# Optimization experiments

Measured on AMD Instinct MI355X. Metric: run time of the kernel, lower is better.

## Reference

```python
import jax, jax.numpy as jnp
import numpy as np

B, N, E_PER_G = 32, 2048, 16384
NF, NHID, NCLS = 128, 128, 10
RATIO = 0.5
NT = B * N
E = B * E_PER_G
K1 = int(np.ceil(RATIO * N))        # 1024 nodes kept per graph after pool1
K2 = int(np.ceil(RATIO * K1))       # 512
K3 = int(np.ceil(RATIO * K2))       # 256


def setup_inputs() -> dict:
    key = jax.random.key(0)
    ks = jax.random.split(key, 16)
    x = jax.random.normal(ks[0], (NT, NF), dtype=jnp.float32)
    off = (jnp.arange(B, dtype=jnp.int32) * N)[:, None]
    src = (jax.random.randint(ks[1], (B, E_PER_G), 0, N, dtype=jnp.int32) + off).reshape(-1)
    dst = (jax.random.randint(ks[2], (B, E_PER_G), 0, N, dtype=jnp.int32) + off).reshape(-1)
    edge_index = jnp.stack([src, dst])
    batch = jnp.repeat(jnp.arange(B, dtype=jnp.int32), N)
    def lin(k, i, o):
        return jax.random.normal(k, (i, o), jnp.float32) / np.float32(np.sqrt(i))
    return {
        'x': x, 'edge_index': edge_index, 'batch': batch,
        'W1': lin(ks[3], NF, NHID), 'b1': jnp.zeros((NHID,), jnp.float32),
        'Wp1': lin(ks[4], NHID, 1), 'bp1': jnp.zeros((1,), jnp.float32),
        'W2': lin(ks[5], NHID, NHID), 'b2': jnp.zeros((NHID,), jnp.float32),
        'Wp2': lin(ks[6], NHID, 1), 'bp2': jnp.zeros((1,), jnp.float32),
        'W3': lin(ks[7], NHID, NHID), 'b3': jnp.zeros((NHID,), jnp.float32),
        'Wp3': lin(ks[8], NHID, 1), 'bp3': jnp.zeros((1,), jnp.float32),
        'lin1_W': lin(ks[9], 2 * NHID, NHID), 'lin1_b': jnp.zeros((NHID,), jnp.float32),
        'lin2_W': lin(ks[10], NHID, NHID // 2), 'lin2_b': jnp.zeros((NHID // 2,), jnp.float32),
        'lin3_W': lin(ks[11], NHID // 2, NCLS), 'lin3_b': jnp.zeros((NCLS,), jnp.float32),
    }


def gcn(x, src, dst, emask, nmask, W, b):
    # PyG GCNConv: add self-loops, symmetric normalization D^-1/2 (A+I) D^-1/2 @ (x W) + b.
    # Removed nodes/edges carry weight 0 via masks (equivalent to filter_adj re-indexing).
    h = x @ W
    deg = jnp.zeros((NT,), h.dtype).at[dst].add(emask) + nmask
    dinv = jnp.where(deg > 0, 1.0, 0.0) * jax.lax.rsqrt(jnp.where(deg > 0, deg, 1.0))
    coef = dinv[src] * dinv[dst] * emask               # [E]
    out = jnp.zeros_like(h).at[dst].add(coef[:, None] * h[src])
    out = out + ((dinv * dinv) * nmask)[:, None] * h   # self-loop term, norm = 1/deg
    return out + b


def sagpool(x, src, dst, emask, nmask, Wp, bp, k):
    # score = GCNConv(nhid,1); keep top-k per graph; x <- x[perm] * tanh(score[perm])
    score = gcn(x, src, dst, emask, nmask, Wp, bp)[:, 0]          # [NT]
    s = jnp.where(nmask > 0, score, -jnp.inf).reshape(B, N)
    _, idx = jax.lax.top_k(s, k)                                   # [B, k]
    keep = jnp.zeros((B, N), x.dtype).at[jnp.arange(B)[:, None], idx].set(1.0).reshape(-1)
    x_new = x * jnp.tanh(score)[:, None] * keep[:, None]
    emask_new = emask * keep[src] * keep[dst]                      # filter_adj
    return x_new, emask_new, keep


def readout(x, nmask, count):
    # [global_max_pool, global_mean_pool] over active nodes of each graph
    xb = x.reshape(B, N, -1)
    m = nmask.reshape(B, N, 1)
    mx = jnp.max(jnp.where(m > 0, xb, -jnp.inf), axis=1)
    mn = jnp.sum(xb * m, axis=1) / count
    return jnp.concatenate([mx, mn], axis=-1)


def reference(x, edge_index, batch, W1, b1, Wp1, bp1, W2, b2, Wp2, bp2,
              W3, b3, Wp3, bp3, lin1_W, lin1_b, lin2_W, lin2_b, lin3_W, lin3_b):
    src, dst = edge_index[0], edge_index[1]
    emask = jnp.ones((E,), x.dtype)
    nmask = jnp.ones((NT,), x.dtype)

    h = jax.nn.relu(gcn(x, src, dst, emask, nmask, W1, b1))
    h, emask, nmask = sagpool(h, src, dst, emask, nmask, Wp1, bp1, K1)
    x1 = readout(h, nmask, jnp.asarray(K1, x.dtype))

    h = jax.nn.relu(gcn(h, src, dst, emask, nmask, W2, b2))
    h, emask, nmask = sagpool(h, src, dst, emask, nmask, Wp2, bp2, K2)
    x2 = readout(h, nmask, jnp.asarray(K2, x.dtype))

    h = jax.nn.relu(gcn(h, src, dst, emask, nmask, W3, b3))
    h, emask, nmask = sagpool(h, src, dst, emask, nmask, Wp3, bp3, K3)
    x3 = readout(h, nmask, jnp.asarray(K3, x.dtype))

    g = x1 + x2 + x3
    g = jax.nn.relu(g @ lin1_W + lin1_b)   # dropout = identity in eval
    g = jax.nn.relu(g @ lin2_W + lin2_b)
    return jax.nn.log_softmax(g @ lin3_W + lin3_b, axis=-1)
```

## Files before the change

kernel.cpp:

```cpp
#include <hip/hip_runtime.h>
#include <math.h>


namespace {

constexpr int B_  = 32;
constexpr int N_  = 2048;
constexpr int NT  = B_ * N_;
constexpr int EPG = 16384;
constexpr int E_  = B_ * EPG;
constexpr int NCLS = 10;
constexpr int AST = 132;

__device__ __forceinline__ int relabel(int bid, int bpgsh) {
  int x = bid & 7, slot = bid >> 3;
  int g = x + 8 * (slot >> bpgsh);
  return (g << bpgsh) + (slot & ((1 << bpgsh) - 1));
}

__device__ void csr_build(const int* __restrict__ src, const int* __restrict__ dst,
                          int* __restrict__ off, int* __restrict__ srcp,
                          float* __restrict__ dinv, float* __restrict__ ds,
                          float* __restrict__ sws, int* hist) {
  const int g = blockIdx.x;
  const int t = threadIdx.x;
  const int base_n = g * N_;
  const int base_e = g * EPG;
  int* wsum8 = hist + 2048;
#pragma unroll
  for (int i = 0; i < 4; ++i) hist[t + 512 * i] = 0;
  __syncthreads();
  for (int i = 0; i < EPG / 512; i += 8) {
    int dd[8];
#pragma unroll
    for (int j = 0; j < 8; ++j) dd[j] = dst[base_e + t + 512 * (i + j)];
#pragma unroll
    for (int j = 0; j < 8; ++j) atomicAdd(&hist[dd[j] - base_n], 1);
  }
  __syncthreads();
  int a[4], ssum = 0;
#pragma unroll
  for (int i = 0; i < 4; ++i) { a[i] = hist[4 * t + i]; ssum += a[i]; }
  {
    int lane = t & 63, w = t >> 6;
    int v = ssum;
#pragma unroll
    for (int o = 1; o < 64; o <<= 1) {
      int nv = __shfl_up(v, o);
      if (lane >= o) v += nv;
    }
    if (lane == 63) wsum8[w] = v;
    __syncthreads();
    if (t == 0) {
      int accv = 0;
      for (int i = 0; i < 8; ++i) { int tmp = wsum8[i]; wsum8[i] = accv; accv += tmp; }
    }
    __syncthreads();
    int run = wsum8[w] + v - ssum;
#pragma unroll
    for (int i = 0; i < 4; ++i) {
      int n = 4 * t + i;
      off[base_n + n] = base_e + run;
      hist[n] = run;
      float d0 = 1.f + (float)a[i];
      float di0 = 1.f / sqrtf(d0);
      dinv[base_n + n] = di0;
      ds[base_n + n] = di0;
      sws[base_n + n] = di0 * di0;
      run += a[i];
    }
    if (g == B_ - 1 && t == 0) off[NT] = E_;
  }
  __syncthreads();
  for (int i = 0; i < EPG / 512; i += 8) {
    int dd[8], ss[8];
#pragma unroll
    for (int j = 0; j < 8; ++j) {
      int e = base_e + t + 512 * (i + j);
      dd[j] = dst[e];
      ss[j] = src[e];
    }
#pragma unroll
    for (int j = 0; j < 8; ++j) {
      int slot = atomicAdd(&hist[dd[j] - base_n], 1);
      srcp[base_e + slot] = ss[j];
    }
  }
}

__global__ __launch_bounds__(512) void k_matmul(const float* __restrict__ A,
                                                const float* __restrict__ W,
                                                float* __restrict__ C,
                                                const int* __restrict__ kept,
                                                int kshift, int bpgsh,
                                                const float* __restrict__ scaleArr,
                                                float* __restrict__ pmx,
                                                float* __restrict__ psm,
                                                const int* __restrict__ src,
                                                const int* __restrict__ dst,
                                                int* __restrict__ off,
                                                int* __restrict__ srcp,
                                                float* __restrict__ dinvW,
                                                float* __restrict__ dsW,
                                                float* __restrict__ swsW,
                                                int csrBlocks) {
  __shared__ float Ast[2][32 * AST];
  __shared__ float Ws[2][32 * 128];
  __shared__ int rowid[128];
  __shared__ float rsc[128];
  if ((int)blockIdx.x < csrBlocks) {
    csr_build(src, dst, off, srcp, dinvW, dsW, swsW, (int*)&Ast[0][0]);
    return;
  }
  const int tid = threadIdx.x;
  const int tile = relabel((int)blockIdx.x - csrBlocks, bpgsh);
  if (kept) {
    if (tid < 128) {
      int q = tile * 128 + tid;
      int g = q >> kshift;
      int row = kept[g * N_ + (q - (g << kshift))];
      rowid[tid] = row;
      rsc[tid] = scaleArr[row];
    }
    __syncthreads();
  }
  const int rowq = tid >> 4;
  const int colq = tid & 15;
  float4 va[2], vw[2];
#pragma unroll
  for (int i = 0; i < 2; ++i) {
    int idx = tid + 512 * i;
    int row = idx >> 3, f4 = idx & 7;
    int grw = kept ? rowid[row] : tile * 128 + row;
    va[i] = *(const float4*)&A[(size_t)grw * 128 + 4 * f4];
  }
#pragma unroll
  for (int i = 0; i < 2; ++i) {
    int idx = tid + 512 * i;
    int kk = idx >> 5, cf = idx & 31;
    vw[i] = *(const float4*)&W[(size_t)kk * 128 + 4 * cf];
  }
#pragma unroll
  for (int i = 0; i < 2; ++i) {
    int idx = tid + 512 * i;
    int row = idx >> 3, f4 = idx & 7;
    Ast[0][(4 * f4 + 0) * AST + row] = va[i].x;
    Ast[0][(4 * f4 + 1) * AST + row] = va[i].y;
    Ast[0][(4 * f4 + 2) * AST + row] = va[i].z;
    Ast[0][(4 * f4 + 3) * AST + row] = va[i].w;
  }
#pragma unroll
  for (int i = 0; i < 2; ++i) {
    int idx = tid + 512 * i;
    int kk = idx >> 5, cf = idx & 31;
    *(float4*)&Ws[0][kk * 128 + 4 * cf] = vw[i];
  }
  __syncthreads();
  float acc[4][8] = {};
  for (int c = 0; c < 4; ++c) {
    int cur = c & 1;
    if (c < 3) {
      int k0n = 32 * (c + 1);
#pragma unroll
      for (int i = 0; i < 2; ++i) {
        int idx = tid + 512 * i;
        int row = idx >> 3, f4 = idx & 7;
        int grw = kept ? rowid[row] : tile * 128 + row;
        va[i] = *(const float4*)&A[(size_t)grw * 128 + k0n + 4 * f4];
      }
#pragma unroll
      for (int i = 0; i < 2; ++i) {
        int idx = tid + 512 * i;
        int kk = idx >> 5, cf = idx & 31;
        vw[i] = *(const float4*)&W[(size_t)(k0n + kk) * 128 + 4 * cf];
      }
    }
#pragma unroll 2
    for (int kk = 0; kk < 32; ++kk) {
      float4 a0 = *(const float4*)&Ast[cur][kk * AST + 4 * rowq];
      float4 w0 = *(const float4*)&Ws[cur][kk * 128 + 4 * colq];
      float4 w1 = *(const float4*)&Ws[cur][kk * 128 + 64 + 4 * colq];
      float a[4] = {a0.x, a0.y, a0.z, a0.w};
      float w[8] = {w0.x, w0.y, w0.z, w0.w, w1.x, w1.y, w1.z, w1.w};
#pragma unroll
      for (int r = 0; r < 4; ++r)
#pragma unroll
        for (int cc = 0; cc < 8; ++cc) acc[r][cc] += a[r] * w[cc];
    }
    if (kept) {
      int kkf = tid >> 4;
      int r0 = (tid & 15) * 8;
      float mxv = -INFINITY, smv = 0.f;
#pragma unroll
      for (int rr = 0; rr < 8; rr += 4) {
        float4 av = *(const float4*)&Ast[cur][kkf * AST + r0 + rr];
        float4 s4 = *(const float4*)&rsc[r0 + rr];
        float v0 = av.x * s4.x, v1 = av.y * s4.y;
        float v2 = av.z * s4.z, v3 = av.w * s4.w;
        mxv = fmaxf(fmaxf(fmaxf(mxv, v0), fmaxf(v1, v2)), v3);
        smv += v0 + v1 + v2 + v3;
      }
#pragma unroll
      for (int o = 8; o >= 1; o >>= 1) {
        mxv = fmaxf(mxv, __shfl_down(mxv, o, 16));
        smv += __shfl_down(smv, o, 16);
      }
      if ((tid & 15) == 0) {
        pmx[(size_t)tile * 128 + 32 * c + kkf] = mxv;
        psm[(size_t)tile * 128 + 32 * c + kkf] = smv;
      }
    }
    if (c < 3) {
      int nxt = cur ^ 1;
#pragma unroll
      for (int i = 0; i < 2; ++i) {
        int idx = tid + 512 * i;
        int row = idx >> 3, f4 = idx & 7;
        Ast[nxt][(4 * f4 + 0) * AST + row] = va[i].x;
        Ast[nxt][(4 * f4 + 1) * AST + row] = va[i].y;
        Ast[nxt][(4 * f4 + 2) * AST + row] = va[i].z;
        Ast[nxt][(4 * f4 + 3) * AST + row] = va[i].w;
      }
#pragma unroll
      for (int i = 0; i < 2; ++i) {
        int idx = tid + 512 * i;
        int kk = idx >> 5, cf = idx & 31;
        *(float4*)&Ws[nxt][kk * 128 + 4 * cf] = vw[i];
      }
      __syncthreads();
    }
  }
#pragma unroll
  for (int r = 0; r < 4; ++r) {
    int grw = kept ? rowid[4 * rowq + r] : tile * 128 + 4 * rowq + r;
    float* Crow = &C[(size_t)grw * 128];
    *(float4*)&Crow[4 * colq] = make_float4(acc[r][0], acc[r][1], acc[r][2], acc[r][3]);
    *(float4*)&Crow[64 + 4 * colq] = make_float4(acc[r][4], acc[r][5], acc[r][6], acc[r][7]);
  }
}

__global__ __launch_bounds__(256) void k_agg(const float4* __restrict__ t4,
                                             const int* __restrict__ off,
                                             const int* __restrict__ srcp,
                                             const float* __restrict__ dinv,
                                             const float* __restrict__ ds,
                                             const float* __restrict__ sws,
                                             const float* __restrict__ bias,
                                             const float* __restrict__ Wp,
                                             float4* __restrict__ h4,
                                             float* __restrict__ t1,
                                             const int* __restrict__ kept,
                                             int kshift, int bpgsh) {
  int q = relabel(blockIdx.x, bpgsh) * 8 + (threadIdx.x >> 5);
  int node;
  if (kept) {
    int g = q >> kshift;
    node = kept[g * N_ + (q - (g << kshift))];
  } else {
    node = q;
  }
  const int lane = threadIdx.x & 31;
  const float dvi = dinv[node];
  float sw = sws[node];
  float4 self = t4[(size_t)node * 32 + lane];
  float4 acc = make_float4(sw * self.x, sw * self.y, sw * self.z, sw * self.w);
  int s = off[node], en = off[node + 1];
  int j = s;
  for (; j + 8 <= en; j += 8) {
    int sv[8];
    float cv[8];
#pragma unroll
    for (int i = 0; i < 8; ++i) sv[i] = srcp[j + i];
#pragma unroll
    for (int i = 0; i < 8; ++i) cv[i] = ds[sv[i]] * dvi;
#pragma unroll
    for (int i = 0; i < 8; ++i) {
      if (cv[i] != 0.f) {
        float4 r = t4[(size_t)sv[i] * 32 + lane];
        acc.x += cv[i] * r.x; acc.y += cv[i] * r.y;
        acc.z += cv[i] * r.z; acc.w += cv[i] * r.w;
      }
    }
  }
  for (; j < en; ++j) {
    int s0 = srcp[j];
    float c0 = ds[s0] * dvi;
    if (c0 != 0.f) {
      float4 r0 = t4[(size_t)s0 * 32 + lane];
      acc.x += c0 * r0.x; acc.y += c0 * r0.y; acc.z += c0 * r0.z; acc.w += c0 * r0.w;
    }
  }
  float4 b4 = ((const float4*)bias)[lane];
  acc.x = fmaxf(acc.x + b4.x, 0.f);
  acc.y = fmaxf(acc.y + b4.y, 0.f);
  acc.z = fmaxf(acc.z + b4.z, 0.f);
  acc.w = fmaxf(acc.w + b4.w, 0.f);
  h4[(size_t)node * 32 + lane] = acc;
  float4 wp = ((const float4*)Wp)[lane];
  float part = acc.x * wp.x + acc.y * wp.y + acc.z * wp.z + acc.w * wp.w;
#pragma unroll
  for (int o = 16; o > 0; o >>= 1) part += __shfl_down(part, o, 32);
  if (lane == 0) t1[node] = part;
}

__global__ __launch_bounds__(1024) void k_pool(const float* __restrict__ t1,
                                               const int* __restrict__ off,
                                               const int* __restrict__ srcp,
                                               float* __restrict__ dinv,
                                               float* __restrict__ ds,
                                               float* __restrict__ sws,
                                               float* __restrict__ scale,
                                               const float* __restrict__ bp,
                                               int* __restrict__ kept,
                                               const float4* __restrict__ h4,
                                               float invk, int k,
                                               const int* __restrict__ inKept, int klen,
                                               const float* __restrict__ pmxA,
                                               const float* __restrict__ psmA,
                                               const float* __restrict__ pmxB,
                                               const float* __restrict__ psmB,
                                               const float* __restrict__ hW1,
                                               const float* __restrict__ hb1,
                                               const float* __restrict__ hW2,
                                               const float* __restrict__ hb2,
                                               const float* __restrict__ hW3,
                                               const float* __restrict__ hb3,
                                               float* __restrict__ out) {
  __shared__ float st1[2048];
  __shared__ float sdv[2048];
  __shared__ float skp[2048];
  __shared__ int skept[1024];
  __shared__ unsigned rephist[4096];
  __shared__ unsigned ebits[64];
  __shared__ int wsum[16];
  __shared__ unsigned bc_digit, bc_prev;
  __shared__ float gr[256], o1[128], o2[64], o3[NCLS];
  const int g = (blockIdx.x & 7) + 8 * (blockIdx.x >> 3);
  const int t = threadIdx.x;
  const int base = g * N_;
  st1[t] = t1[base + t];
  st1[t + 1024] = t1[base + t + 1024];
  sdv[t] = dinv[base + t];
  sdv[t + 1024] = dinv[base + t + 1024];
  skp[t] = 0.f;
  skp[t + 1024] = 0.f;
  if (t < 64) ebits[t] = 0u;
#pragma unroll
  for (int i = 0; i < 4; ++i) rephist[t + 1024 * i] = 0u;
  __syncthreads();
  int nodeq[2] = {-1, -1};
  float raw[2] = {0.f, 0.f};
  unsigned key[2] = {0xFFFFFFFFu, 0xFFFFFFFFu};
  float bpv = bp[0];
#pragma unroll
  for (int q = 0; q < 2; ++q) {
    int i = t + q * 1024;
    if (i >= klen) continue;
    int n = inKept ? (inKept[base + i] - base) : i;
    nodeq[q] = n;
    float di = sdv[n];
    float a = 0.f;
    int s = off[base + n], en = off[base + n + 1];
    int j = s;
    for (; j + 8 <= en; j += 8) {
      int sv[8];
#pragma unroll
      for (int i2 = 0; i2 < 8; ++i2) sv[i2] = srcp[j + i2] - base;
#pragma unroll
      for (int i2 = 0; i2 < 8; ++i2) a += sdv[sv[i2]] * st1[sv[i2]];
    }
    for (; j < en; ++j) {
      int sl = srcp[j] - base;
      a += sdv[sl] * st1[sl];
    }
    raw[q] = di * di * st1[n] + di * a + bpv;
    unsigned u = __float_as_uint(raw[q]);
    u = (u & 0x80000000u) ? ~u : (u | 0x80000000u);
    u = ~u;
    if (di <= 0.f) u = 0xFFFFFFFFu;
    key[q] = u;
  }
  unsigned prefix = 0u, rem = (unsigned)k;
  const int wv = t >> 6;
  for (int shift = 24; shift >= 0; shift -= 8) {
    unsigned mask = (shift == 24) ? 0u : (0xFFFFFFFFu << (shift + 8));
#pragma unroll
    for (int q = 0; q < 2; ++q)
      if (nodeq[q] >= 0 && (key[q] & mask) == prefix)
        atomicAdd(&rephist[(wv << 8) + ((key[q] >> shift) & 255u)], 1u);
    __syncthreads();
    unsigned binv = 0u, v = 0u;
    if (t < 256) {
#pragma unroll
      for (int w = 0; w < 16; ++w) binv += rephist[(w << 8) + t];
      v = binv;
#pragma unroll
      for (int o = 1; o < 64; o <<= 1) {
        unsigned nv = __shfl_up(v, o);
        if ((t & 63) >= o) v += nv;
      }
      if ((t & 63) == 63) wsum[t >> 6] = (int)v;
    }
    __syncthreads();
    if (t < 256) {
      unsigned pre = 0u;
      int w4 = t >> 6;
      for (int u = 0; u < w4; ++u) pre += (unsigned)wsum[u];
      unsigned inc = v + pre, exc = inc - binv;
      if (inc >= rem && exc < rem) { bc_digit = (unsigned)t; bc_prev = exc; }
    }
    __syncthreads();
    if (shift > 0) {
#pragma unroll
      for (int i = 0; i < 4; ++i) rephist[t + 1024 * i] = 0u;
    }
    __syncthreads();
    prefix |= bc_digit << shift;
    rem -= bc_prev;
  }
  const unsigned Tkey = prefix;
  const int need = (int)rem;
#pragma unroll
  for (int q = 0; q < 2; ++q) {
    int n = nodeq[q];
    if (n >= 0 && key[q] == Tkey) atomicOr(&ebits[n >> 5], 1u << (n & 31));
  }
  __syncthreads();
#pragma unroll
  for (int q = 0; q < 2; ++q) {
    int n = nodeq[q];
    if (n < 0) continue;
    float kp;
    if (key[q] < Tkey) {
      kp = 1.f;
    } else if (key[q] == Tkey) {
      int w = n >> 5;
      int rank = __popc(ebits[w] & ((1u << (n & 31)) - 1u));
      for (int u = 0; u < w; ++u) rank += __popc(ebits[u]);
      kp = (rank < need) ? 1.f : 0.f;
    } else {
      kp = 0.f;
    }
    skp[n] = kp;
    float sc = kp * tanhf(raw[q]);
    st1[n] = sc;
    scale[base + n] = sc;
  }
  __syncthreads();
  {
    int lane = t & 63, w = t >> 6;
    int a0 = (int)skp[2 * t], a1 = (int)skp[2 * t + 1];
    int ps = a0 + a1;
    int v = ps;
#pragma unroll
    for (int o = 1; o < 64; o <<= 1) {
      int nv = __shfl_up(v, o);
      if (lane >= o) v += nv;
    }
    if (lane == 63) wsum[w] = v;
    __syncthreads();
    if (t == 0) {
      int accv = 0;
      for (int i = 0; i < 16; ++i) { int tmp = wsum[i]; wsum[i] = accv; accv += tmp; }
    }
    __syncthreads();
    int excl = wsum[w] + v - ps;
    if (a0) { kept[base + excl] = base + 2 * t; skept[excl] = base + 2 * t; }
    if (a1) { kept[base + excl + a0] = base + 2 * t + 1; skept[excl + a0] = base + 2 * t + 1; }
  }
#pragma unroll
  for (int q = 0; q < 2; ++q) {
    int n = nodeq[q];
    if (n < 0) continue;
    float nm = skp[n];
    float d = nm;
    int s = off[base + n], en = off[base + n + 1];
    int j = s;
    for (; j + 8 <= en; j += 8) {
      int sv[8];
#pragma unroll
      for (int i2 = 0; i2 < 8; ++i2) sv[i2] = srcp[j + i2] - base;
#pragma unroll
      for (int i2 = 0; i2 < 8; ++i2) d += skp[sv[i2]];
    }
    for (; j < en; ++j) d += skp[srcp[j] - base];
    float di = (nm > 0.f) ? (1.f / sqrtf(d)) : 0.f;
    float sc = st1[n];
    dinv[base + n] = di;
    ds[base + n] = di * sc;
    sws[base + n] = di * di * sc;
  }
  if (!out) return;
  __syncthreads();
  const int lane = t & 31, ng = t >> 5;
  float4 mx = make_float4(-INFINITY, -INFINITY, -INFINITY, -INFINITY);
  float4 sm = make_float4(0.f, 0.f, 0.f, 0.f);
  for (int i = ng; i < k; i += 32) {
    int node = skept[i];
    float sc = st1[node - base];
    float4 v = h4[(size_t)node * 32 + lane];
    v.x *= sc; v.y *= sc; v.z *= sc; v.w *= sc;
    mx.x = fmaxf(mx.x, v.x); mx.y = fmaxf(mx.y, v.y);
    mx.z = fmaxf(mx.z, v.z); mx.w = fmaxf(mx.w, v.w);
    sm.x += v.x; sm.y += v.y; sm.z += v.z; sm.w += v.w;
  }
  float4* red = (float4*)rephist;
  for (int d = 16; d >= 1; d >>= 1) {
    if (ng >= d && ng < 2 * d) {
      red[(ng - d) * 32 + lane] = mx;
      red[512 + (ng - d) * 32 + lane] = sm;
    }
    __syncthreads();
    if (ng < d) {
      float4 omx = red[ng * 32 + lane];
      float4 osm = red[512 + ng * 32 + lane];
      mx.x = fmaxf(mx.x, omx.x); mx.y = fmaxf(mx.y, omx.y);
      mx.z = fmaxf(mx.z, omx.z); mx.w = fmaxf(mx.w, omx.w);
      sm.x += osm.x; sm.y += osm.y; sm.z += osm.z; sm.w += osm.w;
    }
    __syncthreads();
  }
  if (ng == 0) {
    gr[4 * lane + 0] = mx.x;
    gr[4 * lane + 1] = mx.y;
    gr[4 * lane + 2] = mx.z;
    gr[4 * lane + 3] = mx.w;
    gr[128 + 4 * lane + 0] = sm.x * invk;
    gr[128 + 4 * lane + 1] = sm.y * invk;
    gr[128 + 4 * lane + 2] = sm.z * invk;
    gr[128 + 4 * lane + 3] = sm.w * invk;
  }
  __syncthreads();
  if (t < 128) {
    float mxA = -INFINITY, smA = 0.f;
#pragma unroll
    for (int p = 0; p < 8; ++p) {
      mxA = fmaxf(mxA, pmxA[(size_t)(g * 8 + p) * 128 + t]);
      smA += psmA[(size_t)(g * 8 + p) * 128 + t];
    }
    float mxB = -INFINITY, smB = 0.f;
#pragma unroll
    for (int p = 0; p < 4; ++p) {
      mxB = fmaxf(mxB, pmxB[(size_t)(g * 4 + p) * 128 + t]);
      smB += psmB[(size_t)(g * 4 + p) * 128 + t];
    }
    gr[t] += mxA + mxB;
    gr[t + 128] += smA * (1.f / 1024.f) + smB * (1.f / 512.f);
  }
  __syncthreads();
  if (t < 128) {
    float a = hb1[t];
    for (int kk = 0; kk < 256; ++kk) a += gr[kk] * hW1[kk * 128 + t];
    o1[t] = fmaxf(a, 0.f);
  }
  __syncthreads();
  if (t < 64) {
    float a2 = hb2[t];
    for (int kk = 0; kk < 128; ++kk) a2 += o1[kk] * hW2[kk * 64 + t];
    o2[t] = fmaxf(a2, 0.f);
  }
  __syncthreads();
  if (t < NCLS) {
    float a3 = hb3[t];
    for (int kk = 0; kk < 64; ++kk) a3 += o2[kk] * hW3[kk * NCLS + t];
    o3[t] = a3;
  }
  __syncthreads();
  if (t == 0) {
    float m = -INFINITY;
    for (int c = 0; c < NCLS; ++c) m = fmaxf(m, o3[c]);
    float sum = 0.f;
    for (int c = 0; c < NCLS; ++c) sum += expf(o3[c] - m);
    float lse = logf(sum);
    for (int c = 0; c < NCLS; ++c) out[g * NCLS + c] = o3[c] - m - lse;
  }
}

}

extern "C" void kernel_launch(void* const* d_in, const int* in_sizes, int n_in,
                              void* d_out, int out_size, void* d_ws, size_t ws_size,
                              hipStream_t stream) {
  const float* x = (const float*)d_in[0];
  const int* ei = (const int*)d_in[1];
  const int* src = ei;
  const int* dst = ei + E_;
  const float* Wl[3]  = {(const float*)d_in[3], (const float*)d_in[7], (const float*)d_in[11]};
  const float* bl[3]  = {(const float*)d_in[4], (const float*)d_in[8], (const float*)d_in[12]};
  const float* Wpl[3] = {(const float*)d_in[5], (const float*)d_in[9], (const float*)d_in[13]};
  const float* bpl[3] = {(const float*)d_in[6], (const float*)d_in[10], (const float*)d_in[14]};
  const float* l1W = (const float*)d_in[15];
  const float* l1b = (const float*)d_in[16];
  const float* l2W = (const float*)d_in[17];
  const float* l2b = (const float*)d_in[18];
  const float* l3W = (const float*)d_in[19];
  const float* l3b = (const float*)d_in[20];

  char* p = (char*)d_ws;
  auto alloc = [&](size_t bytes) -> void* {
    void* r = (void*)p;
    p += (bytes + 255) & ~size_t(255);
    return r;
  };
  float* h      = (float*)alloc((size_t)NT * 128 * 4);
  float* t      = (float*)alloc((size_t)NT * 128 * 4);
  float* dinv   = (float*)alloc(NT * 4);
  float* ds     = (float*)alloc(NT * 4);
  float* sws    = (float*)alloc(NT * 4);
  float* scale  = (float*)alloc(NT * 4);
  float* t1     = (float*)alloc(NT * 4);
  int*   srcp   = (int*)alloc(E_ * 4);
  int*   off    = (int*)alloc((NT + 1) * 4);
  int*   kept0  = (int*)alloc(NT * 4);
  int*   kept1  = (int*)alloc(NT * 4);
  int*   kept2  = (int*)alloc(NT * 4);
  float* pmxA   = (float*)alloc(256 * 128 * 4);
  float* psmA   = (float*)alloc(256 * 128 * 4);
  float* pmxB   = (float*)alloc(128 * 128 * 4);
  float* psmB   = (float*)alloc(128 * 128 * 4);

  int* keptL[3] = {kept0, kept1, kept2};
  const int K[3] = {1024, 512, 256};
  const int KSH[3] = {10, 9, 8};
  float* pmxL[3] = {nullptr, pmxA, pmxB};
  float* psmL[3] = {nullptr, psmA, psmB};

  const float* inF = x;
  for (int l = 0; l < 3; ++l) {
    const int* inKept = (l == 0) ? nullptr : keptL[l - 1];
    int inKsh = (l == 0) ? 11 : KSH[l - 1];
    int nrows = (l == 0) ? NT : B_ * K[l - 1];
    int mm_bpgsh = (l == 0) ? 4 : (l == 1 ? 3 : 2);
    int ag_bpgsh = (l == 0) ? 8 : (l == 1 ? 7 : 6);
    int csrB = (l == 0) ? B_ : 0;
    int klen = (l == 0) ? N_ : K[l - 1];
    bool last = (l == 2);
    k_matmul<<<nrows / 128 + csrB, 512, 0, stream>>>(
        inF, Wl[l], t, inKept, inKsh, mm_bpgsh, scale, pmxL[l], psmL[l],
        src, dst, off, srcp, dinv, ds, sws, csrB);
    k_agg<<<nrows / 8, 256, 0, stream>>>((const float4*)t, off, srcp, dinv, ds, sws,
                                         bl[l], Wpl[l], (float4*)h, t1, inKept, inKsh,
                                         ag_bpgsh);
    k_pool<<<B_, 1024, 0, stream>>>(t1, off, srcp, dinv, ds, sws, scale, bpl[l],
                                    keptL[l], (const float4*)h,
                                    1.f / (float)K[l], K[l], inKept, klen,
                                    last ? pmxA : nullptr, last ? psmA : nullptr,
                                    last ? pmxB : nullptr, last ? psmB : nullptr,
                                    l1W, l1b, l2W, l2b, l3W, l3b,
                                    last ? (float*)d_out : nullptr);
    inF = h;
  }
}
```

Before: 296.2 us.

## Split first-layer matmul into dedicated 64-row kernel with 128-thread CSR build

Adds a specialized layer-0 matmul kernel using 64-row tiles, 128 threads, 8x8 per-thread register blocking and K-chunks of 16. The CSR construction is co-scheduled in the same launch but now runs with 128 threads per graph instead of 512. The general matmul kernel drops its unused-layer branches and CSR arguments. The aim is more blocks and better register reuse for the large first GEMM, at the risk of a slower CSR build on fewer threads, which may become the critical path.

```diff
diff --git a/kernel.cpp b/kernel.cpp
--- a/kernel.cpp
+++ b/kernel.cpp
@@ -11,6 +11,7 @@
 constexpr int E_  = B_ * EPG;
 constexpr int NCLS = 10;
 constexpr int AST = 132;
+constexpr int AST64 = 68;
 
 __device__ __forceinline__ int relabel(int bid, int bpgsh) {
   int x = bid & 7, slot = bid >> 3;
@@ -18,29 +19,29 @@
   return (g << bpgsh) + (slot & ((1 << bpgsh) - 1));
 }
 
-__device__ void csr_build(const int* __restrict__ src, const int* __restrict__ dst,
-                          int* __restrict__ off, int* __restrict__ srcp,
-                          float* __restrict__ dinv, float* __restrict__ ds,
-                          float* __restrict__ sws, int* hist) {
+__device__ void csr_build128(const int* __restrict__ src, const int* __restrict__ dst,
+                             int* __restrict__ off, int* __restrict__ srcp,
+                             float* __restrict__ dinv, float* __restrict__ ds,
+                             float* __restrict__ sws, int* hist) {
   const int g = blockIdx.x;
   const int t = threadIdx.x;
   const int base_n = g * N_;
   const int base_e = g * EPG;
-  int* wsum8 = hist + 2048;
-#pragma unroll
-  for (int i = 0; i < 4; ++i) hist[t + 512 * i] = 0;
-  __syncthreads();
-  for (int i = 0; i < EPG / 512; i += 8) {
+  int* wsum2 = hist + 2048;
+#pragma unroll
+  for (int i = 0; i < 16; ++i) hist[t + 128 * i] = 0;
+  __syncthreads();
+  for (int i = 0; i < EPG / 128; i += 8) {
     int dd[8];
 #pragma unroll
-    for (int j = 0; j < 8; ++j) dd[j] = dst[base_e + t + 512 * (i + j)];
+    for (int j = 0; j < 8; ++j) dd[j] = dst[base_e + t + 128 * (i + j)];
 #pragma unroll
     for (int j = 0; j < 8; ++j) atomicAdd(&hist[dd[j] - base_n], 1);
   }
   __syncthreads();
-  int a[4], ssum = 0;
-#pragma unroll
-  for (int i = 0; i < 4; ++i) { a[i] = hist[4 * t + i]; ssum += a[i]; }
+  int a[16], ssum = 0;
+#pragma unroll
+  for (int i = 0; i < 16; ++i) { a[i] = hist[16 * t + i]; ssum += a[i]; }
   {
     int lane = t & 63, w = t >> 6;
     int v = ssum;
@@ -49,17 +50,14 @@
       int nv = __shfl_up(v, o);
       if (lane >= o) v += nv;
     }
-    if (lane == 63) wsum8[w] = v;
-    __syncthreads();
-    if (t == 0) {
-      int accv = 0;
-      for (int i = 0; i < 8; ++i) { int tmp = wsum8[i]; wsum8[i] = accv; accv += tmp; }
-    }
-    __syncthreads();
-    int run = wsum8[w] + v - ssum;
-#pragma unroll
-    for (int i = 0; i < 4; ++i) {
-      int n = 4 * t + i;
+    if (lane == 63) wsum2[w] = v;
+    __syncthreads();
+    if (t == 0) { int t0 = wsum2[0]; wsum2[0] = 0; wsum2[1] = t0; }
+    __syncthreads();
+    int run = wsum2[w] + v - ssum;
+#pragma unroll
+    for (int i = 0; i < 16; ++i) {
+      int n = 16 * t + i;
       off[base_n + n] = base_e + run;
       hist[n] = run;
       float d0 = 1.f + (float)a[i];
@@ -72,11 +70,11 @@
     if (g == B_ - 1 && t == 0) off[NT] = E_;
   }
   __syncthreads();
-  for (int i = 0; i < EPG / 512; i += 8) {
+  for (int i = 0; i < EPG / 128; i += 8) {
     int dd[8], ss[8];
 #pragma unroll
     for (int j = 0; j < 8; ++j) {
-      int e = base_e + t + 512 * (i + j);
+      int e = base_e + t + 128 * (i + j);
       dd[j] = dst[e];
       ss[j] = src[e];
     }
@@ -85,6 +83,115 @@
       int slot = atomicAdd(&hist[dd[j] - base_n], 1);
       srcp[base_e + slot] = ss[j];
     }
+  }
+}
+
+__global__ __launch_bounds__(128) void k_mm0(const float* __restrict__ A,
+                                             const float* __restrict__ W,
+                                             float* __restrict__ C,
+                                             const int* __restrict__ src,
+                                             const int* __restrict__ dst,
+                                             int* __restrict__ off,
+                                             int* __restrict__ srcp,
+                                             float* __restrict__ dinvW,
+                                             float* __restrict__ dsW,
+                                             float* __restrict__ swsW) {
+  __shared__ float Ast[2][16 * AST64];
+  __shared__ float Ws[2][16 * 128];
+  if ((int)blockIdx.x < 32) {
+    csr_build128(src, dst, off, srcp, dinvW, dsW, swsW, (int*)&Ast[0][0]);
+    return;
+  }
+  const int tid = threadIdx.x;
+  const int tile = relabel((int)blockIdx.x - 32, 5);
+  const int row0 = tile * 64;
+  const int rowq = tid >> 4;
+  const int colq = tid & 15;
+  float4 va[2], vw[4];
+#pragma unroll
+  for (int i = 0; i < 2; ++i) {
+    int idx = tid + 128 * i;
+    int r = idx >> 2, f4 = idx & 3;
+    va[i] = *(const float4*)&A[(size_t)(row0 + r) * 128 + 4 * f4];
+  }
+#pragma unroll
+  for (int i = 0; i < 4; ++i) {
+    int idx = tid + 128 * i;
+    int kk = idx >> 5, cf = idx & 31;
+    vw[i] = *(const float4*)&W[(size_t)kk * 128 + 4 * cf];
+  }
+#pragma unroll
+  for (int i = 0; i < 2; ++i) {
+    int idx = tid + 128 * i;
+    int r = idx >> 2, f4 = idx & 3;
+    Ast[0][(4 * f4 + 0) * AST64 + r] = va[i].x;
+    Ast[0][(4 * f4 + 1) * AST64 + r] = va[i].y;
+    Ast[0][(4 * f4 + 2) * AST64 + r] = va[i].z;
+    Ast[0][(4 * f4 + 3) * AST64 + r] = va[i].w;
+  }
+#pragma unroll
+  for (int i = 0; i < 4; ++i) {
+    int idx = tid + 128 * i;
+    int kk = idx >> 5, cf = idx & 31;
+    *(float4*)&Ws[0][kk * 128 + 4 * cf] = vw[i];
+  }
+  __syncthreads();
+  float acc[8][8] = {};
+  for (int c = 0; c < 8; ++c) {
+    int cur = c & 1;
+    if (c < 7) {
+      int k0n = 16 * (c + 1);
+#pragma unroll
+      for (int i = 0; i < 2; ++i) {
+        int idx = tid + 128 * i;
+        int r = idx >> 2, f4 = idx & 3;
+        va[i] = *(const float4*)&A[(size_t)(row0 + r) * 128 + k0n + 4 * f4];
+      }
+#pragma unroll
+      for (int i = 0; i < 4; ++i) {
+        int idx = tid + 128 * i;
+        int kk = idx >> 5, cf = idx & 31;
+        vw[i] = *(const float4*)&W[(size_t)(k0n + kk) * 128 + 4 * cf];
+      }
+    }
+#pragma unroll 2
+    for (int kk = 0; kk < 16; ++kk) {
+      float4 a0 = *(const float4*)&Ast[cur][kk * AST64 + 8 * rowq];
+      float4 a1 = *(const float4*)&Ast[cur][kk * AST64 + 8 * rowq + 4];
+      float4 w0 = *(const float4*)&Ws[cur][kk * 128 + 4 * colq];
+      float4 w1 = *(const float4*)&Ws[cur][kk * 128 + 64 + 4 * colq];
+      float a[8] = {a0.x, a0.y, a0.z, a0.w, a1.x, a1.y, a1.z, a1.w};
+      float w[8] = {w0.x, w0.y, w0.z, w0.w, w1.x, w1.y, w1.z, w1.w};
+#pragma unroll
+      for (int r = 0; r < 8; ++r)
+#pragma unroll
+        for (int cc = 0; cc < 8; ++cc) acc[r][cc] += a[r] * w[cc];
+    }
+    if (c < 7) {
+      int nxt = cur ^ 1;
+#pragma unroll
+      for (int i = 0; i < 2; ++i) {
+        int idx = tid + 128 * i;
+        int r = idx >> 2, f4 = idx & 3;
+        Ast[nxt][(4 * f4 + 0) * AST64 + r] = va[i].x;
+        Ast[nxt][(4 * f4 + 1) * AST64 + r] = va[i].y;
+        Ast[nxt][(4 * f4 + 2) * AST64 + r] = va[i].z;
+        Ast[nxt][(4 * f4 + 3) * AST64 + r] = va[i].w;
+      }
+#pragma unroll
+      for (int i = 0; i < 4; ++i) {
+        int idx = tid + 128 * i;
+        int kk = idx >> 5, cf = idx & 31;
+        *(float4*)&Ws[nxt][kk * 128 + 4 * cf] = vw[i];
+      }
+      __syncthreads();
+    }
+  }
+#pragma unroll
+  for (int r = 0; r < 8; ++r) {
+    float* Crow = &C[(size_t)(row0 + 8 * rowq + r) * 128];
+    *(float4*)&Crow[4 * colq] = make_float4(acc[r][0], acc[r][1], acc[r][2], acc[r][3]);
+    *(float4*)&Crow[64 + 4 * colq] = make_float4(acc[r][4], acc[r][5], acc[r][6], acc[r][7]);
   }
 }
 
@@ -95,35 +202,21 @@
                                                 int kshift, int bpgsh,
                                                 const float* __restrict__ scaleArr,
                                                 float* __restrict__ pmx,
-                                                float* __restrict__ psm,
-                                                const int* __restrict__ src,
-                                                const int* __restrict__ dst,
-                                                int* __restrict__ off,
-                                                int* __restrict__ srcp,
-                                                float* __restrict__ dinvW,
-                                                float* __restrict__ dsW,
-                                                float* __restrict__ swsW,
-                                                int csrBlocks) {
+                                                float* __restrict__ psm) {
   __shared__ float Ast[2][32 * AST];
   __shared__ float Ws[2][32 * 128];
   __shared__ int rowid[128];
   __shared__ float rsc[128];
-  if ((int)blockIdx.x < csrBlocks) {
-    csr_build(src, dst, off, srcp, dinvW, dsW, swsW, (int*)&Ast[0][0]);
-    return;
-  }
   const int tid = threadIdx.x;
-  const int tile = relabel((int)blockIdx.x - csrBlocks, bpgsh);
-  if (kept) {
-    if (tid < 128) {
-      int q = tile * 128 + tid;
-      int g = q >> kshift;
-      int row = kept[g * N_ + (q - (g << kshift))];
-      rowid[tid] = row;
-      rsc[tid] = scaleArr[row];
-    }
-    __syncthreads();
-  }
+  const int tile = relabel((int)blockIdx.x, bpgsh);
+  if (tid < 128) {
+    int q = tile * 128 + tid;
+    int g = q >> kshift;
+    int row = kept[g * N_ + (q - (g << kshift))];
+    rowid[tid] = row;
+    rsc[tid] = scaleArr[row];
+  }
+  __syncthreads();
   const int rowq = tid >> 4;
   const int colq = tid & 15;
   float4 va[2], vw[2];
@@ -131,8 +224,7 @@
   for (int i = 0; i < 2; ++i) {
     int idx = tid + 512 * i;
     int row = idx >> 3, f4 = idx & 7;
-    int grw = kept ? rowid[row] : tile * 128 + row;
-    va[i] = *(const float4*)&A[(size_t)grw * 128 + 4 * f4];
+    va[i] = *(const float4*)&A[(size_t)rowid[row] * 128 + 4 * f4];
   }
 #pragma unroll
   for (int i = 0; i < 2; ++i) {
@@ -165,8 +257,7 @@
       for (int i = 0; i < 2; ++i) {
         int idx = tid + 512 * i;
         int row = idx >> 3, f4 = idx & 7;
-        int grw = kept ? rowid[row] : tile * 128 + row;
-        va[i] = *(const float4*)&A[(size_t)grw * 128 + k0n + 4 * f4];
+        va[i] = *(const float4*)&A[(size_t)rowid[row] * 128 + k0n + 4 * f4];
       }
 #pragma unroll
       for (int i = 0; i < 2; ++i) {
@@ -187,7 +278,7 @@
 #pragma unroll
         for (int cc = 0; cc < 8; ++cc) acc[r][cc] += a[r] * w[cc];
     }
-    if (kept) {
+    {
       int kkf = tid >> 4;
       int r0 = (tid & 15) * 8;
       float mxv = -INFINITY, smv = 0.f;
@@ -232,8 +323,7 @@
   }
 #pragma unroll
   for (int r = 0; r < 4; ++r) {
-    int grw = kept ? rowid[4 * rowq + r] : tile * 128 + 4 * rowq + r;
-    float* Crow = &C[(size_t)grw * 128];
+    float* Crow = &C[(size_t)rowid[4 * rowq + r] * 128];
     *(float4*)&Crow[4 * colq] = make_float4(acc[r][0], acc[r][1], acc[r][2], acc[r][3]);
     *(float4*)&Crow[64 + 4 * colq] = make_float4(acc[r][4], acc[r][5], acc[r][6], acc[r][7]);
   }
@@ -630,14 +720,17 @@
     const int* inKept = (l == 0) ? nullptr : keptL[l - 1];
     int inKsh = (l == 0) ? 11 : KSH[l - 1];
     int nrows = (l == 0) ? NT : B_ * K[l - 1];
-    int mm_bpgsh = (l == 0) ? 4 : (l == 1 ? 3 : 2);
     int ag_bpgsh = (l == 0) ? 8 : (l == 1 ? 7 : 6);
-    int csrB = (l == 0) ? B_ : 0;
     int klen = (l == 0) ? N_ : K[l - 1];
     bool last = (l == 2);
-    k_matmul<<<nrows / 128 + csrB, 512, 0, stream>>>(
-        inF, Wl[l], t, inKept, inKsh, mm_bpgsh, scale, pmxL[l], psmL[l],
-        src, dst, off, srcp, dinv, ds, sws, csrB);
+    if (l == 0) {
+      k_mm0<<<1024 + 32, 128, 0, stream>>>(x, Wl[0], t, src, dst, off, srcp,
+                                           dinv, ds, sws);
+    } else {
+      int mm_bpgsh = (l == 1) ? 3 : 2;
+      k_matmul<<<nrows / 128, 512, 0, stream>>>(
+          inF, Wl[l], t, inKept, inKsh, mm_bpgsh, scale, pmxL[l], psmL[l]);
+    }
     k_agg<<<nrows / 8, 256, 0, stream>>>((const float4*)t, off, srcp, dinv, ds, sws,
                                          bl[l], Wpl[l], (float4*)h, t1, inKept, inKsh,
                                          ag_bpgsh);
```

After: 306.7 us. 3.6% more time.

## Split pool scoring and degree renormalization into grid-wide kernels

Applied to the files above, without the earlier changes.

Edge-scan score aggregation and post-pool degree renormalization move out of the per-graph k_pool kernel, which runs only 32 blocks. They become two new kernels, k_score and k_norm, that use eight lanes per node across many blocks. k_pool now only does top-k selection, compaction and readout, and zeros the normalization arrays for dropped nodes. This spreads the serial per-thread edge loops over the whole GPU, at the cost of two extra launches per layer and global-memory rather than LDS gathers.

```diff
diff --git a/kernel.cpp b/kernel.cpp
--- a/kernel.cpp
+++ b/kernel.cpp
@@ -303,14 +303,70 @@
   if (lane == 0) t1[node] = part;
 }
 
-__global__ __launch_bounds__(1024) void k_pool(const float* __restrict__ t1,
+__global__ __launch_bounds__(256) void k_score(const float* __restrict__ t1,
                                                const int* __restrict__ off,
                                                const int* __restrict__ srcp,
+                                               const float* __restrict__ dinv,
+                                               const float* __restrict__ bp,
+                                               float* __restrict__ raw,
+                                               const int* __restrict__ kept,
+                                               int kshift, int bpgsh) {
+  int q = relabel(blockIdx.x, bpgsh) * 32 + (threadIdx.x >> 3);
+  int node;
+  if (kept) {
+    int g = q >> kshift;
+    node = kept[g * N_ + (q - (g << kshift))];
+  } else {
+    node = q;
+  }
+  const int lane = threadIdx.x & 7;
+  int s = off[node], en = off[node + 1];
+  float a = 0.f;
+  for (int j = s + lane; j < en; j += 8) {
+    int sl = srcp[j];
+    a += dinv[sl] * t1[sl];
+  }
+#pragma unroll
+  for (int o = 4; o >= 1; o >>= 1) a += __shfl_down(a, o, 8);
+  if (lane == 0) {
+    float di = dinv[node];
+    raw[node] = di * di * t1[node] + di * a + bp[0];
+  }
+}
+
+__global__ __launch_bounds__(256) void k_norm(const int* __restrict__ off,
+                                              const int* __restrict__ srcp,
+                                              const float* __restrict__ kpmask,
+                                              const float* __restrict__ scale,
+                                              float* __restrict__ dinv,
+                                              float* __restrict__ ds,
+                                              float* __restrict__ sws,
+                                              const int* __restrict__ kept,
+                                              int kshift, int bpgsh) {
+  int q = relabel(blockIdx.x, bpgsh) * 32 + (threadIdx.x >> 3);
+  int g = q >> kshift;
+  int node = kept[g * N_ + (q - (g << kshift))];
+  const int lane = threadIdx.x & 7;
+  int s = off[node], en = off[node + 1];
+  float d = (lane == 0) ? 1.f : 0.f;
+  for (int j = s + lane; j < en; j += 8) d += kpmask[srcp[j]];
+#pragma unroll
+  for (int o = 4; o >= 1; o >>= 1) d += __shfl_down(d, o, 8);
+  if (lane == 0) {
+    float di = 1.f / sqrtf(d);
+    float sc = scale[node];
+    dinv[node] = di;
+    ds[node] = di * sc;
+    sws[node] = di * di * sc;
+  }
+}
+
+__global__ __launch_bounds__(1024) void k_pool(const float* __restrict__ raw,
                                                float* __restrict__ dinv,
                                                float* __restrict__ ds,
                                                float* __restrict__ sws,
                                                float* __restrict__ scale,
-                                               const float* __restrict__ bp,
+                                               float* __restrict__ kpmask,
                                                int* __restrict__ kept,
                                                const float4* __restrict__ h4,
                                                float invk, int k,
@@ -327,7 +383,6 @@
                                                const float* __restrict__ hb3,
                                                float* __restrict__ out) {
   __shared__ float st1[2048];
-  __shared__ float sdv[2048];
   __shared__ float skp[2048];
   __shared__ int skept[1024];
   __shared__ unsigned rephist[4096];
@@ -338,10 +393,8 @@
   const int g = (blockIdx.x & 7) + 8 * (blockIdx.x >> 3);
   const int t = threadIdx.x;
   const int base = g * N_;
-  st1[t] = t1[base + t];
-  st1[t + 1024] = t1[base + t + 1024];
-  sdv[t] = dinv[base + t];
-  sdv[t + 1024] = dinv[base + t + 1024];
+  st1[t] = 0.f;
+  st1[t + 1024] = 0.f;
   skp[t] = 0.f;
   skp[t + 1024] = 0.f;
   if (t < 64) ebits[t] = 0u;
@@ -349,35 +402,19 @@
   for (int i = 0; i < 4; ++i) rephist[t + 1024 * i] = 0u;
   __syncthreads();
   int nodeq[2] = {-1, -1};
-  float raw[2] = {0.f, 0.f};
+  float rawv[2] = {0.f, 0.f};
   unsigned key[2] = {0xFFFFFFFFu, 0xFFFFFFFFu};
-  float bpv = bp[0];
 #pragma unroll
   for (int q = 0; q < 2; ++q) {
     int i = t + q * 1024;
     if (i >= klen) continue;
     int n = inKept ? (inKept[base + i] - base) : i;
     nodeq[q] = n;
-    float di = sdv[n];
-    float a = 0.f;
-    int s = off[base + n], en = off[base + n + 1];
-    int j = s;
-    for (; j + 8 <= en; j += 8) {
-      int sv[8];
-#pragma unroll
-      for (int i2 = 0; i2 < 8; ++i2) sv[i2] = srcp[j + i2] - base;
-#pragma unroll
-      for (int i2 = 0; i2 < 8; ++i2) a += sdv[sv[i2]] * st1[sv[i2]];
-    }
-    for (; j < en; ++j) {
-      int sl = srcp[j] - base;
-      a += sdv[sl] * st1[sl];
-    }
-    raw[q] = di * di * st1[n] + di * a + bpv;
-    unsigned u = __float_as_uint(raw[q]);
+    float r = raw[base + n];
+    rawv[q] = r;
+    unsigned u = __float_as_uint(r);
     u = (u & 0x80000000u) ? ~u : (u | 0x80000000u);
     u = ~u;
-    if (di <= 0.f) u = 0xFFFFFFFFu;
     key[q] = u;
   }
   unsigned prefix = 0u, rem = (unsigned)k;
@@ -442,9 +479,15 @@
       kp = 0.f;
     }
     skp[n] = kp;
-    float sc = kp * tanhf(raw[q]);
+    float sc = kp * tanhf(rawv[q]);
     st1[n] = sc;
     scale[base + n] = sc;
+    kpmask[base + n] = kp;
+    if (kp == 0.f) {
+      dinv[base + n] = 0.f;
+      ds[base + n] = 0.f;
+      sws[base + n] = 0.f;
+    }
   }
   __syncthreads();
   {
@@ -467,28 +510,6 @@
     int excl = wsum[w] + v - ps;
     if (a0) { kept[base + excl] = base + 2 * t; skept[excl] = base + 2 * t; }
     if (a1) { kept[base + excl + a0] = base + 2 * t + 1; skept[excl + a0] = base + 2 * t + 1; }
-  }
-#pragma unroll
-  for (int q = 0; q < 2; ++q) {
-    int n = nodeq[q];
-    if (n < 0) continue;
-    float nm = skp[n];
-    float d = nm;
-    int s = off[base + n], en = off[base + n + 1];
-    int j = s;
-    for (; j + 8 <= en; j += 8) {
-      int sv[8];
-#pragma unroll
-      for (int i2 = 0; i2 < 8; ++i2) sv[i2] = srcp[j + i2] - base;
-#pragma unroll
-      for (int i2 = 0; i2 < 8; ++i2) d += skp[sv[i2]];
-    }
-    for (; j < en; ++j) d += skp[srcp[j] - base];
-    float di = (nm > 0.f) ? (1.f / sqrtf(d)) : 0.f;
-    float sc = st1[n];
-    dinv[base + n] = di;
-    ds[base + n] = di * sc;
-    sws[base + n] = di * di * sc;
   }
   if (!out) return;
   __syncthreads();
@@ -609,6 +630,8 @@
   float* sws    = (float*)alloc(NT * 4);
   float* scale  = (float*)alloc(NT * 4);
   float* t1     = (float*)alloc(NT * 4);
+  float* raw    = (float*)alloc(NT * 4);
+  float* kpmask = (float*)alloc(NT * 4);
   int*   srcp   = (int*)alloc(E_ * 4);
   int*   off    = (int*)alloc((NT + 1) * 4);
   int*   kept0  = (int*)alloc(NT * 4);
@@ -632,6 +655,8 @@
     int nrows = (l == 0) ? NT : B_ * K[l - 1];
     int mm_bpgsh = (l == 0) ? 4 : (l == 1 ? 3 : 2);
     int ag_bpgsh = (l == 0) ? 8 : (l == 1 ? 7 : 6);
+    int sc_bpgsh = (l == 0) ? 6 : (l == 1 ? 5 : 4);
+    int nm_bpgsh = (l == 0) ? 5 : 4;
     int csrB = (l == 0) ? B_ : 0;
     int klen = (l == 0) ? N_ : K[l - 1];
     bool last = (l == 2);
@@ -641,13 +666,20 @@
     k_agg<<<nrows / 8, 256, 0, stream>>>((const float4*)t, off, srcp, dinv, ds, sws,
                                          bl[l], Wpl[l], (float4*)h, t1, inKept, inKsh,
                                          ag_bpgsh);
-    k_pool<<<B_, 1024, 0, stream>>>(t1, off, srcp, dinv, ds, sws, scale, bpl[l],
+    k_score<<<nrows / 32, 256, 0, stream>>>(t1, off, srcp, dinv, bpl[l], raw,
+                                            inKept, inKsh, sc_bpgsh);
+    k_pool<<<B_, 1024, 0, stream>>>(raw, dinv, ds, sws, scale, kpmask,
                                     keptL[l], (const float4*)h,
                                     1.f / (float)K[l], K[l], inKept, klen,
                                     last ? pmxA : nullptr, last ? psmA : nullptr,
                                     last ? pmxB : nullptr, last ? psmB : nullptr,
                                     l1W, l1b, l2W, l2b, l3W, l3b,
                                     last ? (float*)d_out : nullptr);
+    if (!last) {
+      k_norm<<<(B_ * K[l]) / 32, 256, 0, stream>>>(off, srcp, kpmask, scale,
+                                                   dinv, ds, sws, keptL[l],
+                                                   KSH[l], nm_bpgsh);
+    }
     inF = h;
   }
 }
```

Result: no change. 301.6 us (+1.8%).
